# Optimization experiments

Hardware: AMD Instinct MI355X
Metric: run time of the kernel (lower is better)

Reference implementation:

```python
import jax, jax.numpy as jnp
import numpy as np

N_EXPERTS = 8
TOP_K = 2

# NOTE: dropout is treated as identity (inference/eval mode), matching
# nn.Dropout in eval(). gate_logits returned is post-softmax, exactly as in
# the torch code (it overwrites gate_logits with F.softmax output).

def setup_inputs() -> dict:
    key = jax.random.key(0)
    k1, k2, k3, k4 = jax.random.split(key, 4)
    B, T, S = 32, 512, 512
    x = jax.random.normal(k1, (B, T, S), dtype=jnp.float32)
    gate_w = jax.random.normal(k2, (N_EXPERTS, S), dtype=jnp.float32) * (1.0 / np.sqrt(S))
    expert_w = jax.random.normal(k3, (N_EXPERTS, S, S), dtype=jnp.float32) * (1.0 / np.sqrt(S))
    expert_b = jax.random.normal(k4, (N_EXPERTS, S), dtype=jnp.float32) * 0.01
    return {"x": x, "gate_w": gate_w, "expert_w": expert_w, "expert_b": expert_b}


def reference(x, gate_w, expert_w, expert_b):
    # Gating: Linear(seq_len -> n_experts, no bias) then softmax over experts
    logits = jnp.einsum('bti,ei->bte', x, gate_w)          # [B,T,E]
    gates = jax.nn.softmax(logits, axis=-1)                # [B,T,E]
    # top-k routing weights
    w, sel = jax.lax.top_k(gates, TOP_K)                   # [B,T,K], [B,T,K]
    # dense combine weights: zero except at selected experts
    comb = jnp.sum(jax.nn.one_hot(sel, N_EXPERTS, dtype=x.dtype) * w[..., None], axis=-2)  # [B,T,E]
    # all-expert linear outputs (XLA fuses the weighted combine)
    expert_out = jnp.einsum('bti,eoi->bteo', x, expert_w) + expert_b[None, None]  # [B,T,E,S]
    out = jnp.einsum('bte,bteo->bto', comb, expert_out)    # [B,T,S]
    out = jax.nn.relu(out)
    return (out, gates)
```

## Files before the change

### kernel.cpp

```cpp
#include <hip/hip_runtime.h>
#include <stdint.h>

#define NT 16384
#define SDIM 512
#define NE 8
#define BM 128
#define BN 128
#define BK 32
#define NSTEP (SDIM / BK)
#define NPAIR 28
#define MAX_TILES 156
#define GEMM_GRID (MAX_TILES * 4)

typedef __attribute__((ext_vector_type(8))) short short8v;
typedef __attribute__((ext_vector_type(8))) unsigned short ushort8v;
typedef __attribute__((ext_vector_type(4))) float f32x4;

#define GLOAD_LDS16(gp, lp) __builtin_amdgcn_global_load_lds( \
    (const __attribute__((address_space(1))) uint32_t*)(gp), \
    (__attribute__((address_space(3))) uint32_t*)(lp), 16, 0, 0)

__device__ __forceinline__ unsigned short f2bf(float f) {
  uint32_t x = __float_as_uint(f);
  x = (x + 0x7FFFu + ((x >> 16) & 1u)) >> 16;
  return (unsigned short)x;
}

__global__ __launch_bounds__(256) void gate_conv_kernel(
    const float* __restrict__ x, const float* __restrict__ gw,
    const float* __restrict__ ew,
    unsigned short* __restrict__ xb, unsigned short* __restrict__ wb,
    float* __restrict__ gates_out, float* __restrict__ wts,
    int* __restrict__ sels, int* __restrict__ cnt) {
  if (blockIdx.x == 0 && threadIdx.x < 32) cnt[threadIdx.x] = 0;

  int lane = threadIdx.x & 63;
  int wv = threadIdx.x >> 6;

  float4 ga[NE], gb[NE];
#pragma unroll
  for (int e = 0; e < NE; e++) {
    const float4* g4 = (const float4*)(gw + e * SDIM + lane * 8);
    ga[e] = g4[0]; gb[e] = g4[1];
  }

  int tbase = blockIdx.x * 16 + wv * 4;
#pragma unroll 1
  for (int i = 0; i < 4; i++) {
    int t = tbase + i;
    const float* xr = x + (size_t)t * SDIM;
    float4 xa = ((const float4*)xr)[lane * 2];
    float4 xbv = ((const float4*)xr)[lane * 2 + 1];

    ushort8v u;
    u[0] = f2bf(xa.x); u[1] = f2bf(xa.y); u[2] = f2bf(xa.z); u[3] = f2bf(xa.w);
    u[4] = f2bf(xbv.x); u[5] = f2bf(xbv.y); u[6] = f2bf(xbv.z); u[7] = f2bf(xbv.w);
    *(ushort8v*)(xb + (size_t)t * SDIM + lane * 8) = u;

    double part[NE];
#pragma unroll
    for (int e = 0; e < NE; e++) {
      double s;
      s  = (double)xa.x * ga[e].x;  s += (double)xa.y * ga[e].y;
      s += (double)xa.z * ga[e].z;  s += (double)xa.w * ga[e].w;
      s += (double)xbv.x * gb[e].x; s += (double)xbv.y * gb[e].y;
      s += (double)xbv.z * gb[e].z; s += (double)xbv.w * gb[e].w;
      part[e] = s;
    }
#pragma unroll
    for (int e = 0; e < NE; e++) {
#pragma unroll
      for (int off = 32; off >= 1; off >>= 1)
        part[e] += __shfl_xor(part[e], off, 64);
    }

    float lg[NE];
#pragma unroll
    for (int e = 0; e < NE; e++) lg[e] = (float)part[e];
    float mx = lg[0];
#pragma unroll
    for (int e = 1; e < NE; e++) mx = fmaxf(mx, lg[e]);
    float ex[NE]; float sum = 0.f;
#pragma unroll
    for (int e = 0; e < NE; e++) { ex[e] = expf(lg[e] - mx); sum += ex[e]; }
    float inv = 1.0f / sum;
    float g[NE];
#pragma unroll
    for (int e = 0; e < NE; e++) g[e] = ex[e] * inv;

    int s0 = 0; float v0 = g[0];
#pragma unroll
    for (int e = 1; e < NE; e++) if (g[e] > v0) { v0 = g[e]; s0 = e; }
    int s1 = -1; float v1 = -1.0f;
#pragma unroll
    for (int e = 0; e < NE; e++) if (e != s0 && g[e] > v1) { v1 = g[e]; s1 = e; }

    if (lane == 0) {
      float* go = gates_out + (size_t)t * NE;
#pragma unroll
      for (int e = 0; e < NE; e++) go[e] = g[e];
      wts[t * 2] = v0; wts[t * 2 + 1] = v1;
      sels[t * 2] = s0; sels[t * 2 + 1] = s1;
    }
  }

  int ci = (blockIdx.x * 256 + threadIdx.x) * 8;
  const float4* p = (const float4*)(ew + ci);
  float4 a = p[0], b = p[1];
  ushort8v w;
  w[0] = f2bf(a.x); w[1] = f2bf(a.y); w[2] = f2bf(a.z); w[3] = f2bf(a.w);
  w[4] = f2bf(b.x); w[5] = f2bf(b.y); w[6] = f2bf(b.z); w[7] = f2bf(b.w);
  *(ushort8v*)(wb + ci) = w;
}

__global__ __launch_bounds__(1024) void scatter_kernel(
    const int* __restrict__ sels, int* __restrict__ cnt, int* __restrict__ list) {
  __shared__ int lc[NPAIR];
  __shared__ int lb[NPAIR];
  int tid = threadIdx.x;
  if (tid < NPAIR) lc[tid] = 0;
  __syncthreads();
  int t = blockIdx.x * 1024 + tid;
  int s0 = sels[t * 2], s1 = sels[t * 2 + 1];
  int a = min(s0, s1), b = max(s0, s1);
  int tri = 7 * a - ((a * (a - 1)) >> 1) + (b - a - 1);
  int p = atomicAdd(&lc[tri], 1);
  __syncthreads();
  if (tid < NPAIR) lb[tid] = atomicAdd(cnt + tid, lc[tid]);
  __syncthreads();
  list[tri * NT + lb[tri] + p] = t;
}

__global__ void build_tiles(const int* __restrict__ cnt, int4* __restrict__ desc) {
  int lane = threadIdx.x & 63;
  int c = (lane < NPAIR) ? cnt[lane] : 0;
  int nt = (c + BM - 1) / BM;
  int pre = nt;
#pragma unroll
  for (int off = 1; off < 32; off <<= 1) {
    int v = __shfl_up(pre, off, 64);
    if (lane >= off) pre += v;
  }
  pre -= nt;
  int total = __shfl(pre + nt, NPAIR - 1, 64);
  if (lane < NPAIR) {
    int a = 0, rem = lane;
    while (rem >= 7 - a) { rem -= 7 - a; a++; }
    int b = a + 1 + rem;
    int k = 0;
    for (int s = 0; s < c; s += BM, k++)
      desc[pre + k] = make_int4(a | (b << 8) | (lane << 16), s, min(BM, c - s), 0);
  }
  for (int j = total + lane; j < MAX_TILES; j += 64)
    desc[j] = make_int4(0, 0, 0, 0);
}

__global__ __launch_bounds__(512, 4) void moe_gemm(
    const unsigned short* __restrict__ xb, const unsigned short* __restrict__ wbuf,
    const int* __restrict__ list, const float* __restrict__ wts,
    const int* __restrict__ sels, const int4* __restrict__ desc,
    const float* __restrict__ ebias, float* __restrict__ out) {
  int flat = blockIdx.x;
  int v = (flat & 7) * (GEMM_GRID / 8) + (flat >> 3);
  int tile = v >> 2, nb = v & 3;

  int4 d = desc[tile];
  int rows = d.z;
  if (rows == 0) return;
  int ea = d.x & 255, eb2 = (d.x >> 8) & 255, tri = d.x >> 16;
  int start = d.y;
  int nbase = nb * BN;
  const int* gl = list + tri * NT + start;

  __shared__ unsigned short lA[3][BM * BK];
  __shared__ unsigned short lB[3][2 * BN * BK];

  int tid = threadIdx.x, lane = tid & 63, wv = tid >> 6;

  int pa = tid >> 3, qa = tid & 7;
  int rowA = 2 * pa + (qa >> 2);
  int k16A = (qa & 3) ^ (pa & 3);
  int tokA = (rowA < rows) ? gl[rowA] : gl[0];
  const unsigned short* srcA = xb + (size_t)tokA * SDIM + k16A * 8;

  const unsigned short* srcB[2];
#pragma unroll
  for (int g = 0; g < 2; g++) {
    int c = g * 512 + tid;
    int slot = c >> 9;
    int cc = c & 511;
    int p = cc >> 3, q = cc & 7;
    int row = 2 * p + (q >> 2);
    int k16 = (q & 3) ^ (p & 3);
    int e = slot ? eb2 : ea;
    srcB[g] = wbuf + (size_t)(e * SDIM + nbase + row) * SDIM + k16 * 8;
  }

  char* lAb = (char*)lA;
  char* lBb = (char*)lB;
  int wm = wv >> 1, wn = wv & 1;
  int arow = wm * 32 + (lane & 15);
  int brow = wn * 64 + (lane & 15);
  int kreg = lane >> 4;

  int offA[2], offB[2][4];
#pragma unroll
  for (int mi = 0; mi < 2; mi++) {
    int lr = arow + mi * 16;
    int p = lr >> 1, h = lr & 1;
    offA[mi] = p * 128 + (h * 4 + (kreg ^ (p & 3))) * 16;
  }
#pragma unroll
  for (int s = 0; s < 2; s++)
#pragma unroll
    for (int ni = 0; ni < 4; ni++) {
      int lr = brow + ni * 16;
      int p = lr >> 1, h = lr & 1;
      offB[s][ni] = s * 8192 + p * 128 + (h * 4 + (kreg ^ (p & 3))) * 16;
    }

  f32x4 acc[2][2][4];
#pragma unroll
  for (int s = 0; s < 2; s++)
#pragma unroll
    for (int i = 0; i < 2; i++)
#pragma unroll
      for (int j = 0; j < 4; j++) acc[s][i][j] = (f32x4){0.f, 0.f, 0.f, 0.f};

#define STAGE(st, k0) do { \
    GLOAD_LDS16(srcA + (k0), lAb + (st) * 8192 + tid * 16); \
    _Pragma("unroll") \
    for (int g = 0; g < 2; g++) \
      GLOAD_LDS16(srcB[g] + (k0), lBb + (st) * 16384 + (g * 512 + tid) * 16); \
  } while (0)

#define COMPUTE(st) do { \
    const char* pA = lAb + (st) * 8192; \
    const char* pB = lBb + (st) * 16384; \
    short8v a[2]; \
    _Pragma("unroll") \
    for (int mi = 0; mi < 2; mi++) a[mi] = *(const short8v*)(pA + offA[mi]); \
    _Pragma("unroll") \
    for (int s = 0; s < 2; s++) { \
      short8v b[4]; \
      _Pragma("unroll") \
      for (int ni = 0; ni < 4; ni++) b[ni] = *(const short8v*)(pB + offB[s][ni]); \
      _Pragma("unroll") \
      for (int mi = 0; mi < 2; mi++) \
        _Pragma("unroll") \
        for (int ni = 0; ni < 4; ni++) \
          acc[s][mi][ni] = __builtin_amdgcn_mfma_f32_16x16x32_bf16(a[mi], b[ni], acc[s][mi][ni], 0, 0, 0); \
    } \
  } while (0)

  STAGE(0, 0);
  STAGE(1, BK);
#pragma unroll 1
  for (int t = 0; t < NSTEP; t++) {
    if (t + 2 < NSTEP) {
      STAGE((t + 2) % 3, (t + 2) * BK);
      asm volatile("s_waitcnt vmcnt(6)" ::: "memory");
    } else if (t + 2 == NSTEP) {
      asm volatile("s_waitcnt vmcnt(3)" ::: "memory");
    } else {
      asm volatile("s_waitcnt vmcnt(0)" ::: "memory");
    }
    __builtin_amdgcn_s_barrier();
    __builtin_amdgcn_sched_barrier(0);
    __builtin_amdgcn_s_setprio(1);
    COMPUTE(t % 3);
    __builtin_amdgcn_s_setprio(0);
    __builtin_amdgcn_s_barrier();
  }

  int rg = lane >> 4;
  int ncol = nbase + wn * 64 + (lane & 15);
  float bA[4], bB[4];
#pragma unroll
  for (int ni = 0; ni < 4; ni++) {
    bA[ni] = ebias[ea * SDIM + ncol + ni * 16];
    bB[ni] = ebias[eb2 * SDIM + ncol + ni * 16];
  }
#pragma unroll
  for (int mi = 0; mi < 2; mi++) {
#pragma unroll
    for (int r = 0; r < 4; r++) {
      int m = wm * 32 + mi * 16 + rg * 4 + r;
      if (m < rows) {
        int tok = gl[m];
        float2 wp = *(const float2*)&wts[tok * 2];
        int sA = sels[tok * 2];
        float wA = (sA == ea) ? wp.x : wp.y;
        float wB = (sA == ea) ? wp.y : wp.x;
        float* orow = out + (size_t)tok * SDIM + ncol;
#pragma unroll
        for (int ni = 0; ni < 4; ni++) {
          float vv = wA * (acc[0][mi][ni][r] + bA[ni]) + wB * (acc[1][mi][ni][r] + bB[ni]);
          orow[ni * 16] = fmaxf(vv, 0.f);
        }
      }
    }
  }
#undef STAGE
#undef COMPUTE
}

extern "C" void kernel_launch(void* const* d_in, const int* in_sizes, int n_in,
                              void* d_out, int out_size, void* d_ws, size_t ws_size,
                              hipStream_t stream) {
  const float* x        = (const float*)d_in[0];
  const float* gate_w   = (const float*)d_in[1];
  const float* expert_w = (const float*)d_in[2];
  const float* expert_b = (const float*)d_in[3];
  float* out = (float*)d_out;

  char* ws = (char*)d_ws;
  unsigned short* xb = (unsigned short*)(ws);
  unsigned short* wb = (unsigned short*)(ws + 16777216);
  float* wts  = (float*)(ws + 20971520);
  int* sels   = (int*)(ws + 21102592);
  int* cnt    = (int*)(ws + 21233664);
  int* list   = (int*)(ws + 21233792);
  int4* desc  = (int4*)(ws + 23068800);

  gate_conv_kernel<<<NT / 16, 256, 0, stream>>>(x, gate_w, expert_w, xb, wb,
                                                out + (size_t)NT * SDIM,
                                                wts, sels, cnt);
  scatter_kernel<<<NT / 1024, 1024, 0, stream>>>(sels, cnt, list);
  build_tiles<<<1, 64, 0, stream>>>(cnt, desc);
  moe_gemm<<<GEMM_GRID, 512, 0, stream>>>(xb, wb, list, wts, sels, desc,
                                          expert_b, out);
}
```

Before: 73.80 us.

## Replace tile-descriptor kernel with persistent atomic work queue in MoE GEMM

Removes the build_tiles launch and turns the grouped GEMM into a persistent kernel with 512 blocks. Blocks pull tile indices from an atomic counter stored in the cnt buffer and decode pair, start and row count by scanning the per-pair counts. This removes a kernel launch and the empty blocks of the fixed oversized grid. In exchange it loses the XCD-aware block swizzle, adds an atomic and extra barriers per tile, and relies on the counter slot being reset on every call.

```diff
diff --git a/kernel.cpp b/kernel.cpp
--- a/kernel.cpp
+++ b/kernel.cpp
@@ -9,8 +9,7 @@
 #define BK 32
 #define NSTEP (SDIM / BK)
 #define NPAIR 28
-#define MAX_TILES 156
-#define GEMM_GRID (MAX_TILES * 4)
+#define GEMM_GRID 512
 
 typedef __attribute__((ext_vector_type(8))) short short8v;
 typedef __attribute__((ext_vector_type(8))) unsigned short ushort8v;
@@ -131,71 +130,16 @@
   list[tri * NT + lb[tri] + p] = t;
 }
 
-__global__ void build_tiles(const int* __restrict__ cnt, int4* __restrict__ desc) {
-  int lane = threadIdx.x & 63;
-  int c = (lane < NPAIR) ? cnt[lane] : 0;
-  int nt = (c + BM - 1) / BM;
-  int pre = nt;
-#pragma unroll
-  for (int off = 1; off < 32; off <<= 1) {
-    int v = __shfl_up(pre, off, 64);
-    if (lane >= off) pre += v;
-  }
-  pre -= nt;
-  int total = __shfl(pre + nt, NPAIR - 1, 64);
-  if (lane < NPAIR) {
-    int a = 0, rem = lane;
-    while (rem >= 7 - a) { rem -= 7 - a; a++; }
-    int b = a + 1 + rem;
-    int k = 0;
-    for (int s = 0; s < c; s += BM, k++)
-      desc[pre + k] = make_int4(a | (b << 8) | (lane << 16), s, min(BM, c - s), 0);
-  }
-  for (int j = total + lane; j < MAX_TILES; j += 64)
-    desc[j] = make_int4(0, 0, 0, 0);
-}
-
 __global__ __launch_bounds__(512, 4) void moe_gemm(
     const unsigned short* __restrict__ xb, const unsigned short* __restrict__ wbuf,
     const int* __restrict__ list, const float* __restrict__ wts,
-    const int* __restrict__ sels, const int4* __restrict__ desc,
+    const int* __restrict__ sels, int* __restrict__ cnt,
     const float* __restrict__ ebias, float* __restrict__ out) {
-  int flat = blockIdx.x;
-  int v = (flat & 7) * (GEMM_GRID / 8) + (flat >> 3);
-  int tile = v >> 2, nb = v & 3;
-
-  int4 d = desc[tile];
-  int rows = d.z;
-  if (rows == 0) return;
-  int ea = d.x & 255, eb2 = (d.x >> 8) & 255, tri = d.x >> 16;
-  int start = d.y;
-  int nbase = nb * BN;
-  const int* gl = list + tri * NT + start;
-
   __shared__ unsigned short lA[3][BM * BK];
   __shared__ unsigned short lB[3][2 * BN * BK];
+  __shared__ int sIdx;
 
   int tid = threadIdx.x, lane = tid & 63, wv = tid >> 6;
-
-  int pa = tid >> 3, qa = tid & 7;
-  int rowA = 2 * pa + (qa >> 2);
-  int k16A = (qa & 3) ^ (pa & 3);
-  int tokA = (rowA < rows) ? gl[rowA] : gl[0];
-  const unsigned short* srcA = xb + (size_t)tokA * SDIM + k16A * 8;
-
-  const unsigned short* srcB[2];
-#pragma unroll
-  for (int g = 0; g < 2; g++) {
-    int c = g * 512 + tid;
-    int slot = c >> 9;
-    int cc = c & 511;
-    int p = cc >> 3, q = cc & 7;
-    int row = 2 * p + (q >> 2);
-    int k16 = (q & 3) ^ (p & 3);
-    int e = slot ? eb2 : ea;
-    srcB[g] = wbuf + (size_t)(e * SDIM + nbase + row) * SDIM + k16 * 8;
-  }
-
   char* lAb = (char*)lA;
   char* lBb = (char*)lB;
   int wm = wv >> 1, wn = wv & 1;
@@ -219,13 +163,71 @@
       offB[s][ni] = s * 8192 + p * 128 + (h * 4 + (kreg ^ (p & 3))) * 16;
     }
 
-  f32x4 acc[2][2][4];
-#pragma unroll
-  for (int s = 0; s < 2; s++)
-#pragma unroll
-    for (int i = 0; i < 2; i++)
-#pragma unroll
-      for (int j = 0; j < 4; j++) acc[s][i][j] = (f32x4){0.f, 0.f, 0.f, 0.f};
+  int pa = tid >> 3, qa = tid & 7;
+  int rowA = 2 * pa + (qa >> 2);
+  int k16A = (qa & 3) ^ (pa & 3);
+
+  int brow_g[2], bk16_g[2], bslot_g[2];
+#pragma unroll
+  for (int g = 0; g < 2; g++) {
+    int c = g * 512 + tid;
+    bslot_g[g] = c >> 9;
+    int cc = c & 511;
+    int p = cc >> 3, q = cc & 7;
+    brow_g[g] = 2 * p + (q >> 2);
+    bk16_g[g] = (q & 3) ^ (p & 3);
+  }
+
+  int Wt = 0;
+#pragma unroll 1
+  for (int t = 0; t < NPAIR; t++) Wt += (cnt[t] + BM - 1) / BM;
+  int W = Wt * 4;
+
+#pragma unroll 1
+  while (true) {
+    __syncthreads();
+    if (tid == 0) sIdx = atomicAdd(cnt + 31, 1);
+    __syncthreads();
+    int idx = sIdx;
+    if (idx >= W) break;
+    int tileIdx = idx >> 2, nb = idx & 3;
+
+    int tri = 0, start = 0, rows = 0, ea = 0, eb2 = 1;
+    {
+      int pre = 0, a = 0, b = 1;
+#pragma unroll 1
+      for (int t = 0; t < NPAIR; t++) {
+        int c = cnt[t];
+        int nt = (c + BM - 1) / BM;
+        if (tileIdx < pre + nt) {
+          tri = t; start = (tileIdx - pre) * BM; rows = min(BM, c - start);
+          ea = a; eb2 = b;
+          break;
+        }
+        pre += nt;
+        b++; if (b == NE) { a++; b = a + 1; }
+      }
+    }
+
+    int nbase = nb * BN;
+    const int* gl = list + tri * NT + start;
+
+    int tokA = (rowA < rows) ? gl[rowA] : gl[0];
+    const unsigned short* srcA = xb + (size_t)tokA * SDIM + k16A * 8;
+    const unsigned short* srcB[2];
+#pragma unroll
+    for (int g = 0; g < 2; g++) {
+      int e = bslot_g[g] ? eb2 : ea;
+      srcB[g] = wbuf + (size_t)(e * SDIM + nbase + brow_g[g]) * SDIM + bk16_g[g] * 8;
+    }
+
+    f32x4 acc[2][2][4];
+#pragma unroll
+    for (int s = 0; s < 2; s++)
+#pragma unroll
+      for (int i = 0; i < 2; i++)
+#pragma unroll
+        for (int j = 0; j < 4; j++) acc[s][i][j] = (f32x4){0.f, 0.f, 0.f, 0.f};
 
 #define STAGE(st, k0) do { \
     GLOAD_LDS16(srcA + (k0), lAb + (st) * 8192 + tid * 16); \
@@ -253,56 +255,57 @@
     } \
   } while (0)
 
-  STAGE(0, 0);
-  STAGE(1, BK);
-#pragma unroll 1
-  for (int t = 0; t < NSTEP; t++) {
-    if (t + 2 < NSTEP) {
-      STAGE((t + 2) % 3, (t + 2) * BK);
-      asm volatile("s_waitcnt vmcnt(6)" ::: "memory");
-    } else if (t + 2 == NSTEP) {
-      asm volatile("s_waitcnt vmcnt(3)" ::: "memory");
-    } else {
-      asm volatile("s_waitcnt vmcnt(0)" ::: "memory");
-    }
-    __builtin_amdgcn_s_barrier();
-    __builtin_amdgcn_sched_barrier(0);
-    __builtin_amdgcn_s_setprio(1);
-    COMPUTE(t % 3);
-    __builtin_amdgcn_s_setprio(0);
-    __builtin_amdgcn_s_barrier();
-  }
-
-  int rg = lane >> 4;
-  int ncol = nbase + wn * 64 + (lane & 15);
-  float bA[4], bB[4];
-#pragma unroll
-  for (int ni = 0; ni < 4; ni++) {
-    bA[ni] = ebias[ea * SDIM + ncol + ni * 16];
-    bB[ni] = ebias[eb2 * SDIM + ncol + ni * 16];
-  }
-#pragma unroll
-  for (int mi = 0; mi < 2; mi++) {
-#pragma unroll
-    for (int r = 0; r < 4; r++) {
-      int m = wm * 32 + mi * 16 + rg * 4 + r;
-      if (m < rows) {
-        int tok = gl[m];
-        float2 wp = *(const float2*)&wts[tok * 2];
-        int sA = sels[tok * 2];
-        float wA = (sA == ea) ? wp.x : wp.y;
-        float wB = (sA == ea) ? wp.y : wp.x;
-        float* orow = out + (size_t)tok * SDIM + ncol;
-#pragma unroll
-        for (int ni = 0; ni < 4; ni++) {
-          float vv = wA * (acc[0][mi][ni][r] + bA[ni]) + wB * (acc[1][mi][ni][r] + bB[ni]);
-          orow[ni * 16] = fmaxf(vv, 0.f);
+    STAGE(0, 0);
+    STAGE(1, BK);
+#pragma unroll 1
+    for (int t = 0; t < NSTEP; t++) {
+      if (t + 2 < NSTEP) {
+        STAGE((t + 2) % 3, (t + 2) * BK);
+        asm volatile("s_waitcnt vmcnt(6)" ::: "memory");
+      } else if (t + 2 == NSTEP) {
+        asm volatile("s_waitcnt vmcnt(3)" ::: "memory");
+      } else {
+        asm volatile("s_waitcnt vmcnt(0)" ::: "memory");
+      }
+      __builtin_amdgcn_s_barrier();
+      __builtin_amdgcn_sched_barrier(0);
+      __builtin_amdgcn_s_setprio(1);
+      COMPUTE(t % 3);
+      __builtin_amdgcn_s_setprio(0);
+      __builtin_amdgcn_s_barrier();
+    }
+
+    int rg = lane >> 4;
+    int ncol = nbase + wn * 64 + (lane & 15);
+    float bA[4], bB[4];
+#pragma unroll
+    for (int ni = 0; ni < 4; ni++) {
+      bA[ni] = ebias[ea * SDIM + ncol + ni * 16];
+      bB[ni] = ebias[eb2 * SDIM + ncol + ni * 16];
+    }
+#pragma unroll
+    for (int mi = 0; mi < 2; mi++) {
+#pragma unroll
+      for (int r = 0; r < 4; r++) {
+        int m = wm * 32 + mi * 16 + rg * 4 + r;
+        if (m < rows) {
+          int tok = gl[m];
+          float2 wp = *(const float2*)&wts[tok * 2];
+          int sA = sels[tok * 2];
+          float wA = (sA == ea) ? wp.x : wp.y;
+          float wB = (sA == ea) ? wp.y : wp.x;
+          float* orow = out + (size_t)tok * SDIM + ncol;
+#pragma unroll
+          for (int ni = 0; ni < 4; ni++) {
+            float vv = wA * (acc[0][mi][ni][r] + bA[ni]) + wB * (acc[1][mi][ni][r] + bB[ni]);
+            orow[ni * 16] = fmaxf(vv, 0.f);
+          }
         }
       }
     }
-  }
 #undef STAGE
 #undef COMPUTE
+  }
 }
 
 extern "C" void kernel_launch(void* const* d_in, const int* in_sizes, int n_in,
@@ -321,13 +324,11 @@
   int* sels   = (int*)(ws + 21102592);
   int* cnt    = (int*)(ws + 21233664);
   int* list   = (int*)(ws + 21233792);
-  int4* desc  = (int4*)(ws + 23068800);
 
   gate_conv_kernel<<<NT / 16, 256, 0, stream>>>(x, gate_w, expert_w, xb, wb,
                                                 out + (size_t)NT * SDIM,
                                                 wts, sels, cnt);
   scatter_kernel<<<NT / 1024, 1024, 0, stream>>>(sels, cnt, list);
-  build_tiles<<<1, 64, 0, stream>>>(cnt, desc);
-  moe_gemm<<<GEMM_GRID, 512, 0, stream>>>(xb, wb, list, wts, sels, desc,
+  moe_gemm<<<GEMM_GRID, 512, 0, stream>>>(xb, wb, list, wts, sels, cnt,
                                           expert_b, out);
 }
```

New measurement: 96.03 us. 30.1% more time.
